# Kernel tuning notes

Measured on AMD Instinct MI355X. Metric: run time of the kernel, lower is better.

## Reference

```python
import jax, jax.numpy as jnp
import numpy as np

HEADS = 8
EPS = 1e-4

def pixel_norm(x):
    # faithful to source: mean over dim=1 (token axis for [B,T,C] tensors)
    return x / jnp.sqrt(jnp.mean(x * x, axis=1, keepdims=True) + EPS)

def setup_inputs() -> dict:
    key = jax.random.key(0)
    ks = jax.random.split(key, 6)
    B, T, C = 4, 2048, 512
    s = 1.0 / np.sqrt(C)
    return {
        "hidden_states": jax.random.normal(ks[0], (B, T, C), jnp.float32),
        "Wq": jax.random.normal(ks[1], (C, C), jnp.float32) * s,
        "Wk": jax.random.normal(ks[2], (C, C), jnp.float32) * s,
        "Wv": jax.random.normal(ks[3], (C, C), jnp.float32) * s,
        "Wo": jax.random.normal(ks[4], (C, C), jnp.float32) * s,
        "bo": jnp.zeros((C,), jnp.float32),
    }

def reference(hidden_states, Wq, Wk, Wv, Wo, bo):
    B, T, C = hidden_states.shape
    H = HEADS
    d = C // H
    scale = 1.0 / np.sqrt(d)  # attn.scale = head_dim**-0.5
    residual = hidden_states

    q = pixel_norm(hidden_states @ Wq)  # [B,T,C]
    k = pixel_norm(hidden_states @ Wk)
    v = pixel_norm(hidden_states @ Wv)

    # head_to_batch_dim: [B,T,C] -> [B,H,T,d]
    def split_heads(x):
        return x.reshape(B, T, H, d).transpose(0, 2, 1, 3)
    q, k, v = split_heads(q), split_heads(k), split_heads(v)

    scores = jnp.einsum("bhqd,bhkd->bhqk", q, k) * scale
    probs = jax.nn.softmax(scores, axis=-1)
    out = jnp.einsum("bhqk,bhkd->bhqd", probs, v)  # [B,H,T,d]

    # batch_to_head_dim: [B,H,T,d] -> [B,T,C]
    out = out.transpose(0, 2, 1, 3).reshape(B, T, C)
    out = out @ Wo + bo  # to_out[0]; to_out[1] is dropout (identity in eval)
    out = out + residual  # residual_connection
    return out  # rescale_output_factor = 1.0
```

## Files before the change

kernel.cpp:

```cpp
#include <hip/hip_runtime.h>

#define Tt 2048
#define Cc 512
#define Bb 4
#define BC (Bb * Cc)

typedef __attribute__((ext_vector_type(4))) float f32x4;
typedef __attribute__((ext_vector_type(8))) _Float16 f16x8;
typedef __attribute__((ext_vector_type(4))) _Float16 f16x4;

__global__ __launch_bounds__(256) void wsetup(
    const float* __restrict__ Wq, const float* __restrict__ Wk,
    const float* __restrict__ Wv, const float* __restrict__ Wo,
    _Float16* __restrict__ Wt)
{
    const int z = blockIdx.y;
    const float* W = (z == 0) ? Wq : (z == 1) ? Wk : (z == 2) ? Wv : Wo;
    const int k0 = (blockIdx.x >> 3) * 64, n0 = (blockIdx.x & 7) * 64;
    const int tid = threadIdx.x;
    __shared__ float tile[64][65];

#pragma unroll
    for (int i = 0; i < 4; ++i) {
        const int idx = i * 256 + tid;
        const int kr = idx >> 4, c4 = idx & 15;
        float4 v = *(const float4*)&W[(size_t)(k0 + kr) * Cc + n0 + c4 * 4];
        tile[kr][c4 * 4 + 0] = v.x; tile[kr][c4 * 4 + 1] = v.y;
        tile[kr][c4 * 4 + 2] = v.z; tile[kr][c4 * 4 + 3] = v.w;
    }
    __syncthreads();
#pragma unroll
    for (int i = 0; i < 4; ++i) {
        const int idx = i * 256 + tid;
        const int nr = idx >> 4, k4 = idx & 15;
        f16x4 o;
        o[0] = (_Float16)tile[k4 * 4 + 0][nr];
        o[1] = (_Float16)tile[k4 * 4 + 1][nr];
        o[2] = (_Float16)tile[k4 * 4 + 2][nr];
        o[3] = (_Float16)tile[k4 * 4 + 3][nr];
        *(f16x4*)&Wt[((size_t)(z * 512 + n0 + nr)) * Cc + k0 + k4 * 4] = o;
    }
}

__global__ __launch_bounds__(256, 3) void qkv_mfma(
    const float* __restrict__ HS, const _Float16* __restrict__ Wt,
    _Float16* __restrict__ Qf, _Float16* __restrict__ Kf,
    _Float16* __restrict__ Vf, float* __restrict__ colsum)
{
    const int mt = blockIdx.x;
    const int nt = blockIdx.y;
    const int z  = blockIdx.z;
    _Float16* Out = (z == 0) ? Qf : (z == 1) ? Kf : Vf;

    const int tid = threadIdx.x;
    const int wave = tid >> 6, lane = tid & 63;
    const int quad = lane >> 4, lm = lane & 15;
    const int wm = (wave & 1) * 64, wn = (wave >> 1) * 64;

    __shared__ _Float16 sA[128 * 40];
    __shared__ _Float16 sB[128 * 40];

    f32x4 acc[4][4];
#pragma unroll
    for (int mf = 0; mf < 4; ++mf)
#pragma unroll
        for (int nf = 0; nf < 4; ++nf) acc[mf][nf] = (f32x4){0.f, 0.f, 0.f, 0.f};

    const int r2 = tid >> 1, kc = (tid & 1) * 16;
    const float* ga = HS + (size_t)(mt * 128 + r2) * Cc + kc;
    const _Float16* gb = Wt + ((size_t)(z * 512 + nt * 128 + r2)) * Cc + kc;

    for (int k0 = 0; k0 < Cc; k0 += 32) {
        __syncthreads();
        {
            float4 a0 = *(const float4*)&ga[k0];
            float4 a1 = *(const float4*)&ga[k0 + 4];
            float4 a2 = *(const float4*)&ga[k0 + 8];
            float4 a3 = *(const float4*)&ga[k0 + 12];
            f16x8 h0, h1;
            h0[0] = (_Float16)a0.x; h0[1] = (_Float16)a0.y;
            h0[2] = (_Float16)a0.z; h0[3] = (_Float16)a0.w;
            h0[4] = (_Float16)a1.x; h0[5] = (_Float16)a1.y;
            h0[6] = (_Float16)a1.z; h0[7] = (_Float16)a1.w;
            h1[0] = (_Float16)a2.x; h1[1] = (_Float16)a2.y;
            h1[2] = (_Float16)a2.z; h1[3] = (_Float16)a2.w;
            h1[4] = (_Float16)a3.x; h1[5] = (_Float16)a3.y;
            h1[6] = (_Float16)a3.z; h1[7] = (_Float16)a3.w;
            *(f16x8*)&sA[r2 * 40 + kc]     = h0;
            *(f16x8*)&sA[r2 * 40 + kc + 8] = h1;
            *(f16x8*)&sB[r2 * 40 + kc]     = *(const f16x8*)&gb[k0];
            *(f16x8*)&sB[r2 * 40 + kc + 8] = *(const f16x8*)&gb[k0 + 8];
        }
        __syncthreads();

        f16x8 ah[4], bh[4];
#pragma unroll
        for (int mf = 0; mf < 4; ++mf)
            ah[mf] = *(const f16x8*)&sA[(wm + mf * 16 + lm) * 40 + quad * 8];
#pragma unroll
        for (int nf = 0; nf < 4; ++nf)
            bh[nf] = *(const f16x8*)&sB[(wn + nf * 16 + lm) * 40 + quad * 8];
#pragma unroll
        for (int mf = 0; mf < 4; ++mf)
#pragma unroll
            for (int nf = 0; nf < 4; ++nf)
                acc[mf][nf] = __builtin_amdgcn_mfma_f32_16x16x32_f16(ah[mf], bh[nf], acc[mf][nf], 0, 0, 0);
    }

    const int bidx = mt >> 4;
#pragma unroll
    for (int nf = 0; nf < 4; ++nf) {
        float cs = 0.f;
#pragma unroll
        for (int mf = 0; mf < 4; ++mf)
#pragma unroll
            for (int r = 0; r < 4; ++r) {
                const float v = acc[mf][nf][r];
                const size_t idx =
                    (size_t)(mt * 128 + wm + mf * 16 + quad * 4 + r) * Cc +
                    nt * 128 + wn + nf * 16 + lm;
                Out[idx] = (_Float16)v;
                cs += v * v;
            }
        cs += __shfl_xor(cs, 16, 64);
        cs += __shfl_xor(cs, 32, 64);
        if (lane < 16)
            atomicAdd(&colsum[(size_t)z * BC + bidx * Cc + nt * 128 + wn + nf * 16 + lane], cs);
    }
}

__global__ void inv_norm_kernel(const float* __restrict__ colsum,
                                float* __restrict__ inv)
{
    const int i = blockIdx.x * blockDim.x + threadIdx.x;
    if (i < 3 * BC) inv[i] = rsqrtf(colsum[i] * (1.0f / Tt) + 1e-4f);
}

__global__ __launch_bounds__(256) void norm_vt(
    const _Float16* __restrict__ V, _Float16* __restrict__ VT)
{
    const int blk = blockIdx.x;
    const int b = blk >> 8, ct = (blk >> 5) & 7, tt = blk & 31;
    const int t0 = tt * 64, c0 = ct * 64;
    const int tid = threadIdx.x;

    __shared__ _Float16 tile[64 * 72];

#pragma unroll
    for (int i = 0; i < 2; ++i) {
        const int idx = i * 256 + tid;
        const int tr = idx >> 3, c8 = (idx & 7) * 8;
        *(f16x8*)&tile[tr * 72 + c8] =
            *(const f16x8*)&V[(size_t)(b * Tt + t0 + tr) * Cc + c0 + c8];
    }
    __syncthreads();
#pragma unroll
    for (int i = 0; i < 2; ++i) {
        const int idx = i * 256 + tid;
        const int cr = idx >> 3, t8 = (idx & 7) * 8;
        f16x8 o;
#pragma unroll
        for (int j = 0; j < 8; ++j) o[j] = tile[(t8 + j) * 72 + cr];
        *(f16x8*)&VT[(size_t)(b * Cc + c0 + cr) * Tt + t0 + t8] = o;
    }
}

#define LSTR 72

__global__ __launch_bounds__(256, 2) void attn_mfma(
    const _Float16* __restrict__ Qf, const _Float16* __restrict__ Kf,
    const _Float16* __restrict__ VT, const float* __restrict__ inv,
    _Float16* __restrict__ AO)
{
    const int qt = blockIdx.x;
    const int bh = blockIdx.y;
    const int b = bh >> 3, h = bh & 7;
    const int tid = threadIdx.x;
    const int wave = tid >> 6, lane = tid & 63;
    const int quad = lane >> 4, lm = lane & 15;

    __shared__ _Float16 sK[64 * LSTR];
    __shared__ _Float16 sVT[64 * LSTR];
    __shared__ _Float16 sP[4 * 32 * LSTR];
    _Float16* myP = sP + wave * 32 * LSTR;

    f16x8 qb[2][2];
    {
        const float* iqp = inv + b * Cc + h * 64;
        const float* ikp = inv + BC + b * Cc + h * 64;
#pragma unroll
        for (int qf = 0; qf < 2; ++qf) {
            const int row = qt * 128 + wave * 32 + qf * 16 + lm;
#pragma unroll
            for (int ks = 0; ks < 2; ++ks) {
                const int d0 = ks * 32 + quad * 8;
                f16x8 qv = *(const f16x8*)&Qf[(size_t)(b * Tt + row) * Cc + h * 64 + d0];
#pragma unroll
                for (int j = 0; j < 8; ++j) {
                    const float f = (float)qv[j] * iqp[d0 + j] * ikp[d0 + j] * 0.125f;
                    qb[qf][ks][j] = (_Float16)f;
                }
            }
        }
    }

    f32x4 o[4][2];
#pragma unroll
    for (int cf = 0; cf < 4; ++cf)
#pragma unroll
        for (int qf = 0; qf < 2; ++qf) o[cf][qf] = (f32x4){0.f, 0.f, 0.f, 0.f};
    float ls[2] = {0.f, 0.f};

    const int sr0 = tid >> 3, sc0 = (tid & 7) * 8;
    const int sr1 = sr0 + 32;
    const _Float16* gK = Kf + (size_t)b * Tt * Cc + h * 64;
    const _Float16* gV = VT + ((size_t)b * Cc + h * 64) * Tt;

    f16x8 rk0, rk1, rv0, rv1;
    {
        rk0 = *(const f16x8*)&gK[(size_t)sr0 * Cc + sc0];
        rk1 = *(const f16x8*)&gK[(size_t)sr1 * Cc + sc0];
        rv0 = *(const f16x8*)&gV[(size_t)sr0 * Tt + sc0];
        rv1 = *(const f16x8*)&gV[(size_t)sr1 * Tt + sc0];
    }

    for (int kt = 0; kt < 32; ++kt) {
        __syncthreads();
        *(f16x8*)&sK[sr0 * LSTR + sc0] = rk0;
        *(f16x8*)&sK[sr1 * LSTR + sc0] = rk1;
        *(f16x8*)&sVT[sr0 * LSTR + sc0] = rv0;
        *(f16x8*)&sVT[sr1 * LSTR + sc0] = rv1;
        __syncthreads();

        if (kt < 31) {
            const int t0 = (kt + 1) * 64;
            rk0 = *(const f16x8*)&gK[(size_t)(t0 + sr0) * Cc + sc0];
            rk1 = *(const f16x8*)&gK[(size_t)(t0 + sr1) * Cc + sc0];
            rv0 = *(const f16x8*)&gV[(size_t)sr0 * Tt + t0 + sc0];
            rv1 = *(const f16x8*)&gV[(size_t)sr1 * Tt + t0 + sc0];
        }

        f32x4 st[4][2];
#pragma unroll
        for (int kf = 0; kf < 4; ++kf)
#pragma unroll
            for (int qf = 0; qf < 2; ++qf) st[kf][qf] = (f32x4){0.f, 0.f, 0.f, 0.f};
#pragma unroll
        for (int ks = 0; ks < 2; ++ks) {
            f16x8 ka[4];
#pragma unroll
            for (int kf = 0; kf < 4; ++kf)
                ka[kf] = *(const f16x8*)&sK[(kf * 16 + lm) * LSTR + ks * 32 + quad * 8];
#pragma unroll
            for (int kf = 0; kf < 4; ++kf)
#pragma unroll
                for (int qf = 0; qf < 2; ++qf)
                    st[kf][qf] = __builtin_amdgcn_mfma_f32_16x16x32_f16(ka[kf], qb[qf][ks], st[kf][qf], 0, 0, 0);
        }

#pragma unroll
        for (int kf = 0; kf < 4; ++kf)
#pragma unroll
            for (int qf = 0; qf < 2; ++qf) {
                f16x4 pk;
#pragma unroll
                for (int r = 0; r < 4; ++r) {
                    const float p = __expf(st[kf][qf][r]);
                    ls[qf] += p;
                    pk[r] = (_Float16)p;
                }
                *(f16x4*)&myP[(qf * 16 + lm) * LSTR + kf * 16 + quad * 4] = pk;
            }

#pragma unroll
        for (int ks = 0; ks < 2; ++ks) {
            f16x8 pb[2];
#pragma unroll
            for (int qf = 0; qf < 2; ++qf)
                pb[qf] = *(const f16x8*)&myP[(qf * 16 + lm) * LSTR + ks * 32 + quad * 8];
            f16x8 va[4];
#pragma unroll
            for (int cf = 0; cf < 4; ++cf)
                va[cf] = *(const f16x8*)&sVT[(cf * 16 + lm) * LSTR + ks * 32 + quad * 8];
#pragma unroll
            for (int cf = 0; cf < 4; ++cf)
#pragma unroll
                for (int qf = 0; qf < 2; ++qf)
                    o[cf][qf] = __builtin_amdgcn_mfma_f32_16x16x32_f16(va[cf], pb[qf], o[cf][qf], 0, 0, 0);
        }
    }

    float il[2];
#pragma unroll
    for (int qf = 0; qf < 2; ++qf) {
        float s = ls[qf];
        s += __shfl_xor(s, 16, 64);
        s += __shfl_xor(s, 32, 64);
        il[qf] = 1.0f / s;
    }
    const float* ivp = inv + 2 * BC + b * Cc + h * 64;
    float iv[4][4];
#pragma unroll
    for (int cf = 0; cf < 4; ++cf) {
        float4 t = *(const float4*)&ivp[cf * 16 + quad * 4];
        iv[cf][0] = t.x; iv[cf][1] = t.y; iv[cf][2] = t.z; iv[cf][3] = t.w;
    }
#pragma unroll
    for (int qf = 0; qf < 2; ++qf) {
        const size_t row = (size_t)(b * Tt + qt * 128 + wave * 32 + qf * 16 + lm);
#pragma unroll
        for (int cf = 0; cf < 4; ++cf) {
            f16x4 pk;
#pragma unroll
            for (int r = 0; r < 4; ++r)
                pk[r] = (_Float16)(o[cf][qf][r] * il[qf] * iv[cf][r]);
            *(f16x4*)&AO[row * Cc + h * 64 + cf * 16 + quad * 4] = pk;
        }
    }
}

__global__ __launch_bounds__(256, 2) void out_mfma(
    const _Float16* __restrict__ AO, const _Float16* __restrict__ Wt,
    const float* __restrict__ bo, const float* __restrict__ HS,
    float* __restrict__ Outp)
{
    const int mt = blockIdx.x;
    const int nt = blockIdx.y;
    const int tid = threadIdx.x;
    const int wave = tid >> 6, lane = tid & 63;
    const int quad = lane >> 4, lm = lane & 15;
    const int wm = (wave & 1) * 32, wn = (wave >> 1) * 64;

    __shared__ _Float16 sA[64 * 40];
    __shared__ _Float16 sB[128 * 40];

    f32x4 acc[2][4];
#pragma unroll
    for (int mf = 0; mf < 2; ++mf)
#pragma unroll
        for (int nf = 0; nf < 4; ++nf) acc[mf][nf] = (f32x4){0.f, 0.f, 0.f, 0.f};

    const int ra = tid >> 2, ka = (tid & 3) * 8;
    const int rb = tid >> 1, kb = (tid & 1) * 16;
    const _Float16* gah = AO + (size_t)(mt * 64 + ra) * Cc + ka;
    const _Float16* gbh = Wt + ((size_t)(3 * 512 + nt * 128 + rb)) * Cc + kb;

    for (int k0 = 0; k0 < Cc; k0 += 32) {
        __syncthreads();
        {
            *(f16x8*)&sA[ra * 40 + ka] = *(const f16x8*)&gah[k0];
            *(f16x8*)&sB[rb * 40 + kb]     = *(const f16x8*)&gbh[k0];
            *(f16x8*)&sB[rb * 40 + kb + 8] = *(const f16x8*)&gbh[k0 + 8];
        }
        __syncthreads();

        f16x8 ah[2], bh[4];
#pragma unroll
        for (int mf = 0; mf < 2; ++mf)
            ah[mf] = *(const f16x8*)&sA[(wm + mf * 16 + lm) * 40 + quad * 8];
#pragma unroll
        for (int nf = 0; nf < 4; ++nf)
            bh[nf] = *(const f16x8*)&sB[(wn + nf * 16 + lm) * 40 + quad * 8];
#pragma unroll
        for (int mf = 0; mf < 2; ++mf)
#pragma unroll
            for (int nf = 0; nf < 4; ++nf)
                acc[mf][nf] = __builtin_amdgcn_mfma_f32_16x16x32_f16(ah[mf], bh[nf], acc[mf][nf], 0, 0, 0);
    }

#pragma unroll
    for (int mf = 0; mf < 2; ++mf)
#pragma unroll
        for (int r = 0; r < 4; ++r) {
            const size_t m = (size_t)(mt * 64 + wm + mf * 16 + quad * 4 + r);
#pragma unroll
            for (int nf = 0; nf < 4; ++nf) {
                const int col = nt * 128 + wn + nf * 16 + lm;
                Outp[m * Cc + col] = acc[mf][nf][r] + bo[col] + HS[m * Cc + col];
            }
        }
}

extern "C" void kernel_launch(void* const* d_in, const int* in_sizes, int n_in,
                              void* d_out, int out_size, void* d_ws,
                              size_t ws_size, hipStream_t stream)
{
    const float* HS = (const float*)d_in[0];
    const float* Wq = (const float*)d_in[1];
    const float* Wk = (const float*)d_in[2];
    const float* Wv = (const float*)d_in[3];
    const float* Wo = (const float*)d_in[4];
    const float* bo = (const float*)d_in[5];
    float* out = (float*)d_out;

    const size_t SZ = (size_t)Bb * Tt * Cc;
    _Float16* Qf  = (_Float16*)d_ws;
    _Float16* Kf  = Qf + SZ;
    _Float16* Vf  = Kf + SZ;
    _Float16* VTh = Vf + SZ;
    _Float16* AO  = VTh + SZ;
    _Float16* Wt  = AO + SZ;
    float* colsum = (float*)(Wt + 4 * Cc * Cc);
    float* inv    = colsum + 3 * BC;

    hipMemsetAsync(colsum, 0, 3 * BC * sizeof(float), stream);

    wsetup<<<dim3(64, 4), 256, 0, stream>>>(Wq, Wk, Wv, Wo, Wt);

    qkv_mfma<<<dim3(64, 4, 3), 256, 0, stream>>>(HS, Wt, Qf, Kf, Vf, colsum);

    inv_norm_kernel<<<(3 * BC + 255) / 256, 256, 0, stream>>>(colsum, inv);

    norm_vt<<<1024, 256, 0, stream>>>(Vf, VTh);

    attn_mfma<<<dim3(16, 32), 256, 0, stream>>>(Qf, Kf, VTh, inv, AO);

    out_mfma<<<dim3(128, 4), 256, 0, stream>>>(AO, Wt, bo, HS, out);
}
```

Before: 185.0 us.

## Fuse norm and V transpose into QKV GEMM, load K/V directly to registers

The QKV GEMM now writes V already transposed and stores per-tile column sum-of-squares partials, which removes the memset, atomics, the inv_norm kernel and the separate transpose kernel. The attention kernel reduces those partials into shared-memory inverse norms. It drops the LDS staging and barriers for K/V and reads MFMA fragments straight from global memory. It also folds log2e into the Q scale so it can use exp2f, and reorders the grid so heads of one query tile run together. The risk is uncoalesced direct global loads and scattered transposed stores replacing the shared-memory staging, plus redundant partial reductions in every attention block.

Result: slower. 258.1 us (+39.5%).

```diff
diff --git a/kernel.cpp b/kernel.cpp
--- a/kernel.cpp
+++ b/kernel.cpp
@@ -45,12 +45,11 @@
 __global__ __launch_bounds__(256, 3) void qkv_mfma(
     const float* __restrict__ HS, const _Float16* __restrict__ Wt,
     _Float16* __restrict__ Qf, _Float16* __restrict__ Kf,
-    _Float16* __restrict__ Vf, float* __restrict__ colsum)
+    _Float16* __restrict__ VT, float* __restrict__ colpart)
 {
     const int mt = blockIdx.x;
     const int nt = blockIdx.y;
     const int z  = blockIdx.z;
-    _Float16* Out = (z == 0) ? Qf : (z == 1) ? Kf : Vf;
 
     const int tid = threadIdx.x;
     const int wave = tid >> 6, lane = tid & 63;
@@ -59,6 +58,7 @@
 
     __shared__ _Float16 sA[128 * 40];
     __shared__ _Float16 sB[128 * 40];
+    __shared__ float sCS[4][64];
 
     f32x4 acc[4][4];
 #pragma unroll
@@ -107,61 +107,42 @@
                 acc[mf][nf] = __builtin_amdgcn_mfma_f32_16x16x32_f16(ah[mf], bh[nf], acc[mf][nf], 0, 0, 0);
     }
 
-    const int bidx = mt >> 4;
+    const int bidx = mt >> 4, ii = mt & 15;
 #pragma unroll
     for (int nf = 0; nf < 4; ++nf) {
         float cs = 0.f;
-#pragma unroll
-        for (int mf = 0; mf < 4; ++mf)
+        const int c = nt * 128 + wn + nf * 16 + lm;
+#pragma unroll
+        for (int mf = 0; mf < 4; ++mf) {
+            f16x4 pk;
 #pragma unroll
             for (int r = 0; r < 4; ++r) {
                 const float v = acc[mf][nf][r];
-                const size_t idx =
-                    (size_t)(mt * 128 + wm + mf * 16 + quad * 4 + r) * Cc +
-                    nt * 128 + wn + nf * 16 + lm;
-                Out[idx] = (_Float16)v;
                 cs += v * v;
+                pk[r] = (_Float16)v;
             }
+            if (z == 2) {
+                const int tb = ii * 128 + wm + mf * 16 + quad * 4;
+                *(f16x4*)&VT[((size_t)bidx * Cc + c) * Tt + tb] = pk;
+            } else {
+                _Float16* Out = (z == 0) ? Qf : Kf;
+                const size_t m = (size_t)(mt * 128 + wm + mf * 16 + quad * 4);
+                Out[(m + 0) * Cc + c] = pk[0];
+                Out[(m + 1) * Cc + c] = pk[1];
+                Out[(m + 2) * Cc + c] = pk[2];
+                Out[(m + 3) * Cc + c] = pk[3];
+            }
+        }
         cs += __shfl_xor(cs, 16, 64);
         cs += __shfl_xor(cs, 32, 64);
-        if (lane < 16)
-            atomicAdd(&colsum[(size_t)z * BC + bidx * Cc + nt * 128 + wn + nf * 16 + lane], cs);
-    }
-}
-
-__global__ void inv_norm_kernel(const float* __restrict__ colsum,
-                                float* __restrict__ inv)
-{
-    const int i = blockIdx.x * blockDim.x + threadIdx.x;
-    if (i < 3 * BC) inv[i] = rsqrtf(colsum[i] * (1.0f / Tt) + 1e-4f);
-}
-
-__global__ __launch_bounds__(256) void norm_vt(
-    const _Float16* __restrict__ V, _Float16* __restrict__ VT)
-{
-    const int blk = blockIdx.x;
-    const int b = blk >> 8, ct = (blk >> 5) & 7, tt = blk & 31;
-    const int t0 = tt * 64, c0 = ct * 64;
-    const int tid = threadIdx.x;
-
-    __shared__ _Float16 tile[64 * 72];
-
-#pragma unroll
-    for (int i = 0; i < 2; ++i) {
-        const int idx = i * 256 + tid;
-        const int tr = idx >> 3, c8 = (idx & 7) * 8;
-        *(f16x8*)&tile[tr * 72 + c8] =
-            *(const f16x8*)&V[(size_t)(b * Tt + t0 + tr) * Cc + c0 + c8];
+        if (lane < 16) sCS[wave][nf * 16 + lane] = cs;
     }
     __syncthreads();
-#pragma unroll
-    for (int i = 0; i < 2; ++i) {
-        const int idx = i * 256 + tid;
-        const int cr = idx >> 3, t8 = (idx & 7) * 8;
-        f16x8 o;
-#pragma unroll
-        for (int j = 0; j < 8; ++j) o[j] = tile[(t8 + j) * 72 + cr];
-        *(f16x8*)&VT[(size_t)(b * Cc + c0 + cr) * Tt + t0 + t8] = o;
+    if (tid < 128) {
+        const int c = tid;
+        const int wp = c >> 6;
+        const float s = sCS[wp * 2][c & 63] + sCS[wp * 2 + 1][c & 63];
+        colpart[(((size_t)z * 4 + bidx) * 16 + ii) * Cc + nt * 128 + c] = s;
     }
 }
 
@@ -169,38 +150,43 @@
 
 __global__ __launch_bounds__(256, 2) void attn_mfma(
     const _Float16* __restrict__ Qf, const _Float16* __restrict__ Kf,
-    const _Float16* __restrict__ VT, const float* __restrict__ inv,
+    const _Float16* __restrict__ VT, const float* __restrict__ colpart,
     _Float16* __restrict__ AO)
 {
-    const int qt = blockIdx.x;
-    const int bh = blockIdx.y;
+    const int blk = blockIdx.x;
+    const int bh = blk & 31, qt = blk >> 5;
     const int b = bh >> 3, h = bh & 7;
     const int tid = threadIdx.x;
     const int wave = tid >> 6, lane = tid & 63;
     const int quad = lane >> 4, lm = lane & 15;
 
-    __shared__ _Float16 sK[64 * LSTR];
-    __shared__ _Float16 sVT[64 * LSTR];
     __shared__ _Float16 sP[4 * 32 * LSTR];
+    __shared__ float sInv[192];
     _Float16* myP = sP + wave * 32 * LSTR;
 
+    if (tid < 192) {
+        const int z = tid >> 6, cr = tid & 63;
+        const float* cp = colpart + (((size_t)z * 4 + b) * 16) * Cc + h * 64 + cr;
+        float s = 0.f;
+#pragma unroll
+        for (int i = 0; i < 16; ++i) s += cp[(size_t)i * Cc];
+        sInv[tid] = rsqrtf(s * (1.0f / Tt) + 1e-4f);
+    }
+    __syncthreads();
+
+    const float QSC = 0.125f * 1.44269504088896f;
     f16x8 qb[2][2];
-    {
-        const float* iqp = inv + b * Cc + h * 64;
-        const float* ikp = inv + BC + b * Cc + h * 64;
-#pragma unroll
-        for (int qf = 0; qf < 2; ++qf) {
-            const int row = qt * 128 + wave * 32 + qf * 16 + lm;
-#pragma unroll
-            for (int ks = 0; ks < 2; ++ks) {
-                const int d0 = ks * 32 + quad * 8;
-                f16x8 qv = *(const f16x8*)&Qf[(size_t)(b * Tt + row) * Cc + h * 64 + d0];
-#pragma unroll
-                for (int j = 0; j < 8; ++j) {
-                    const float f = (float)qv[j] * iqp[d0 + j] * ikp[d0 + j] * 0.125f;
-                    qb[qf][ks][j] = (_Float16)f;
-                }
-            }
+#pragma unroll
+    for (int qf = 0; qf < 2; ++qf) {
+        const int row = qt * 128 + wave * 32 + qf * 16 + lm;
+#pragma unroll
+        for (int ks = 0; ks < 2; ++ks) {
+            const int d0 = ks * 32 + quad * 8;
+            f16x8 qv = *(const f16x8*)&Qf[(size_t)(b * Tt + row) * Cc + h * 64 + d0];
+#pragma unroll
+            for (int j = 0; j < 8; ++j)
+                qb[qf][ks][j] =
+                    (_Float16)((float)qv[j] * sInv[d0 + j] * sInv[64 + d0 + j] * QSC);
         }
     }
 
@@ -211,34 +197,25 @@
         for (int qf = 0; qf < 2; ++qf) o[cf][qf] = (f32x4){0.f, 0.f, 0.f, 0.f};
     float ls[2] = {0.f, 0.f};
 
-    const int sr0 = tid >> 3, sc0 = (tid & 7) * 8;
-    const int sr1 = sr0 + 32;
     const _Float16* gK = Kf + (size_t)b * Tt * Cc + h * 64;
     const _Float16* gV = VT + ((size_t)b * Cc + h * 64) * Tt;
 
-    f16x8 rk0, rk1, rv0, rv1;
-    {
-        rk0 = *(const f16x8*)&gK[(size_t)sr0 * Cc + sc0];
-        rk1 = *(const f16x8*)&gK[(size_t)sr1 * Cc + sc0];
-        rv0 = *(const f16x8*)&gV[(size_t)sr0 * Tt + sc0];
-        rv1 = *(const f16x8*)&gV[(size_t)sr1 * Tt + sc0];
-    }
-
     for (int kt = 0; kt < 32; ++kt) {
-        __syncthreads();
-        *(f16x8*)&sK[sr0 * LSTR + sc0] = rk0;
-        *(f16x8*)&sK[sr1 * LSTR + sc0] = rk1;
-        *(f16x8*)&sVT[sr0 * LSTR + sc0] = rv0;
-        *(f16x8*)&sVT[sr1 * LSTR + sc0] = rv1;
-        __syncthreads();
-
-        if (kt < 31) {
-            const int t0 = (kt + 1) * 64;
-            rk0 = *(const f16x8*)&gK[(size_t)(t0 + sr0) * Cc + sc0];
-            rk1 = *(const f16x8*)&gK[(size_t)(t0 + sr1) * Cc + sc0];
-            rv0 = *(const f16x8*)&gV[(size_t)sr0 * Tt + t0 + sc0];
-            rv1 = *(const f16x8*)&gV[(size_t)sr1 * Tt + t0 + sc0];
-        }
+        const int t0 = kt * 64;
+
+        f16x8 ka[4][2], va[4][2];
+#pragma unroll
+        for (int kf = 0; kf < 4; ++kf)
+#pragma unroll
+            for (int ks = 0; ks < 2; ++ks)
+                ka[kf][ks] = *(const f16x8*)
+                    &gK[(size_t)(t0 + kf * 16 + lm) * Cc + ks * 32 + quad * 8];
+#pragma unroll
+        for (int cf = 0; cf < 4; ++cf)
+#pragma unroll
+            for (int ks = 0; ks < 2; ++ks)
+                va[cf][ks] = *(const f16x8*)
+                    &gV[(size_t)(cf * 16 + lm) * Tt + t0 + ks * 32 + quad * 8];
 
         f32x4 st[4][2];
 #pragma unroll
@@ -246,17 +223,13 @@
 #pragma unroll
             for (int qf = 0; qf < 2; ++qf) st[kf][qf] = (f32x4){0.f, 0.f, 0.f, 0.f};
 #pragma unroll
-        for (int ks = 0; ks < 2; ++ks) {
-            f16x8 ka[4];
+        for (int ks = 0; ks < 2; ++ks)
 #pragma unroll
             for (int kf = 0; kf < 4; ++kf)
-                ka[kf] = *(const f16x8*)&sK[(kf * 16 + lm) * LSTR + ks * 32 + quad * 8];
-#pragma unroll
-            for (int kf = 0; kf < 4; ++kf)
 #pragma unroll
                 for (int qf = 0; qf < 2; ++qf)
-                    st[kf][qf] = __builtin_amdgcn_mfma_f32_16x16x32_f16(ka[kf], qb[qf][ks], st[kf][qf], 0, 0, 0);
-        }
+                    st[kf][qf] = __builtin_amdgcn_mfma_f32_16x16x32_f16(
+                        ka[kf][ks], qb[qf][ks], st[kf][qf], 0, 0, 0);
 
 #pragma unroll
         for (int kf = 0; kf < 4; ++kf)
@@ -265,7 +238,7 @@
                 f16x4 pk;
 #pragma unroll
                 for (int r = 0; r < 4; ++r) {
-                    const float p = __expf(st[kf][qf][r]);
+                    const float p = exp2f(st[kf][qf][r]);
                     ls[qf] += p;
                     pk[r] = (_Float16)p;
                 }
@@ -278,15 +251,12 @@
 #pragma unroll
             for (int qf = 0; qf < 2; ++qf)
                 pb[qf] = *(const f16x8*)&myP[(qf * 16 + lm) * LSTR + ks * 32 + quad * 8];
-            f16x8 va[4];
 #pragma unroll
             for (int cf = 0; cf < 4; ++cf)
-                va[cf] = *(const f16x8*)&sVT[(cf * 16 + lm) * LSTR + ks * 32 + quad * 8];
-#pragma unroll
-            for (int cf = 0; cf < 4; ++cf)
 #pragma unroll
                 for (int qf = 0; qf < 2; ++qf)
-                    o[cf][qf] = __builtin_amdgcn_mfma_f32_16x16x32_f16(va[cf], pb[qf], o[cf][qf], 0, 0, 0);
+                    o[cf][qf] = __builtin_amdgcn_mfma_f32_16x16x32_f16(
+                        va[cf][ks], pb[qf], o[cf][qf], 0, 0, 0);
         }
     }
 
@@ -298,13 +268,6 @@
         s += __shfl_xor(s, 32, 64);
         il[qf] = 1.0f / s;
     }
-    const float* ivp = inv + 2 * BC + b * Cc + h * 64;
-    float iv[4][4];
-#pragma unroll
-    for (int cf = 0; cf < 4; ++cf) {
-        float4 t = *(const float4*)&ivp[cf * 16 + quad * 4];
-        iv[cf][0] = t.x; iv[cf][1] = t.y; iv[cf][2] = t.z; iv[cf][3] = t.w;
-    }
 #pragma unroll
     for (int qf = 0; qf < 2; ++qf) {
         const size_t row = (size_t)(b * Tt + qt * 128 + wave * 32 + qf * 16 + lm);
@@ -313,7 +276,8 @@
             f16x4 pk;
 #pragma unroll
             for (int r = 0; r < 4; ++r)
-                pk[r] = (_Float16)(o[cf][qf][r] * il[qf] * iv[cf][r]);
+                pk[r] = (_Float16)(o[cf][qf][r] * il[qf] *
+                                   sInv[128 + cf * 16 + quad * 4 + r]);
             *(f16x4*)&AO[row * Cc + h * 64 + cf * 16 + quad * 4] = pk;
         }
     }
@@ -396,24 +360,16 @@
     const size_t SZ = (size_t)Bb * Tt * Cc;
     _Float16* Qf  = (_Float16*)d_ws;
     _Float16* Kf  = Qf + SZ;
-    _Float16* Vf  = Kf + SZ;
-    _Float16* VTh = Vf + SZ;
+    _Float16* VTh = Kf + SZ;
     _Float16* AO  = VTh + SZ;
     _Float16* Wt  = AO + SZ;
-    float* colsum = (float*)(Wt + 4 * Cc * Cc);
-    float* inv    = colsum + 3 * BC;
-
-    hipMemsetAsync(colsum, 0, 3 * BC * sizeof(float), stream);
+    float* colpart = (float*)(Wt + 4 * Cc * Cc);
 
     wsetup<<<dim3(64, 4), 256, 0, stream>>>(Wq, Wk, Wv, Wo, Wt);
 
-    qkv_mfma<<<dim3(64, 4, 3), 256, 0, stream>>>(HS, Wt, Qf, Kf, Vf, colsum);
-
-    inv_norm_kernel<<<(3 * BC + 255) / 256, 256, 0, stream>>>(colsum, inv);
-
-    norm_vt<<<1024, 256, 0, stream>>>(Vf, VTh);
-
-    attn_mfma<<<dim3(16, 32), 256, 0, stream>>>(Qf, Kf, VTh, inv, AO);
+    qkv_mfma<<<dim3(64, 4, 3), 256, 0, stream>>>(HS, Wt, Qf, Kf, VTh, colpart);
+
+    attn_mfma<<<512, 256, 0, stream>>>(Qf, Kf, VTh, colpart, AO);
 
     out_mfma<<<dim3(128, 4), 256, 0, stream>>>(AO, Wt, bo, HS, out);
 }
```
